# Kernel optimization log

Measured on AMD Instinct MI355X. Metric: run time of the kernel, lower is better.

Reference implementation:

```python
import jax, jax.numpy as jnp
import numpy as np


def setup_inputs() -> dict:
    key = jax.random.key(0)
    k1, k2, k3, k4 = jax.random.split(key, 4)
    B, C, K = 8192, 32000, 100
    return {
        "logits": jax.random.normal(k1, (B, C), dtype=jnp.float32),
        "targets": jax.random.randint(k2, (B,), 0, C, dtype=jnp.int32),
        "text_keys": jax.random.randint(k3, (B,), 0, K, dtype=jnp.int32),
        "class_weight_table": jax.random.uniform(k4, (K, C), dtype=jnp.float32),
    }


def reference(logits, targets, text_keys, class_weight_table):
    # per-sample cross entropy: -log_softmax(logits)[i, targets[i]]
    logp = jax.nn.log_softmax(logits, axis=-1)            # [B, C]
    B = logits.shape[0]
    ce = -jnp.take_along_axis(logp, targets[:, None], axis=-1)[:, 0]  # [B]
    # weight lookup: class_weight[text_key][target]
    w = class_weight_table[text_keys, targets]            # [B]
    return jnp.mean(ce * w)
```

## Files before the change

### kernel.cpp

```cpp
#include <hip/hip_runtime.h>
#include <math.h>


#define L2E 1.44269504088896340736f
#define LN2 0.69314718055994530942f

__device__ __forceinline__ float e2x(float x) {
    return __builtin_amdgcn_exp2f(x * L2E);
}
__device__ __forceinline__ float acc4(float4 v) {
    return (e2x(v.x) + e2x(v.y)) + (e2x(v.z) + e2x(v.w));
}

__global__ __launch_bounds__(256) void row_loss_kernel(
    const float* __restrict__ logits,
    const int*   __restrict__ targets,
    const int*   __restrict__ text_keys,
    const float* __restrict__ wtab,
    float*       __restrict__ row_out,
    int C)
{
    const int row = blockIdx.x;
    const float* rowp = logits + (size_t)row * (size_t)C;
    const int tid = threadIdx.x;

    float xt = 0.0f, wgt = 0.0f;
    if (tid == 0) {
        const int t = targets[row];
        xt  = rowp[t];
        wgt = wtab[(size_t)text_keys[row] * (size_t)C + t];
    }

    const int nvec = C >> 2;
    const float4* rowv = (const float4*)rowp;

    float s0 = 0.0f, s1 = 0.0f, s2 = 0.0f, s3 = 0.0f;

    const int full = nvec >> 10;
    int i = tid;
    if (full > 0) {
        float4 a = rowv[i];
        float4 b = rowv[i + 256];
        float4 c = rowv[i + 512];
        float4 d = rowv[i + 768];
        #pragma unroll 1
        for (int it = 1; it < full; ++it) {
            i += 1024;
            float4 a2 = rowv[i];
            float4 b2 = rowv[i + 256];
            float4 c2 = rowv[i + 512];
            float4 d2 = rowv[i + 768];
            s0 += acc4(a); s1 += acc4(b); s2 += acc4(c); s3 += acc4(d);
            a = a2; b = b2; c = c2; d = d2;
        }
        s0 += acc4(a); s1 += acc4(b); s2 += acc4(c); s3 += acc4(d);
        i += 1024;
    }
    for (; i < nvec; i += 256) s0 += acc4(rowv[i]);
    for (int j = (nvec << 2) + tid; j < C; j += 256) s1 += e2x(rowp[j]);

    float s = (s0 + s1) + (s2 + s3);
    #pragma unroll
    for (int off = 32; off > 0; off >>= 1)
        s += __shfl_down(s, off, 64);

    __shared__ float sm[4];
    const int wave = tid >> 6;
    const int lane = tid & 63;
    if (lane == 0) sm[wave] = s;
    __syncthreads();
    if (tid == 0) {
        const float S = (sm[0] + sm[1]) + (sm[2] + sm[3]);
        const float lse = __builtin_amdgcn_logf(S) * LN2;
        row_out[row] = (lse - xt) * wgt;
    }
}

__global__ __launch_bounds__(256) void reduce_mean_kernel(
    const float* __restrict__ row_out, float* __restrict__ out, int B)
{
    const int tid = threadIdx.x;
    float acc = 0.0f;
    for (int i = tid; i < B; i += 256) acc += row_out[i];
    #pragma unroll
    for (int off = 32; off > 0; off >>= 1)
        acc += __shfl_down(acc, off, 64);
    __shared__ float sa[4];
    const int wave = tid >> 6;
    const int lane = tid & 63;
    if (lane == 0) sa[wave] = acc;
    __syncthreads();
    if (tid == 0) {
        out[0] = (sa[0] + sa[1] + sa[2] + sa[3]) / (float)B;
    }
}

extern "C" void kernel_launch(void* const* d_in, const int* in_sizes, int n_in,
                              void* d_out, int out_size, void* d_ws, size_t ws_size,
                              hipStream_t stream) {
    const float* logits    = (const float*)d_in[0];
    const int*   targets   = (const int*)d_in[1];
    const int*   text_keys = (const int*)d_in[2];
    const float* wtab      = (const float*)d_in[3];
    float* out    = (float*)d_out;
    float* row_ws = (float*)d_ws;

    const int B = in_sizes[1];
    const int C = in_sizes[0] / B;

    row_loss_kernel<<<B, 256, 0, stream>>>(logits, targets, text_keys, wtab,
                                           row_ws, C);
    reduce_mean_kernel<<<1, 256, 0, stream>>>(row_ws, out, B);
}
```

Baseline: 1.300 ms.

## Assign one wavefront per row and use nontemporal vector loads

Each 64-lane wavefront now processes a full row, with four rows per 256-thread block. This removes the shared-memory reduction and the block barrier. The per-row loop now issues four nontemporal float4 loads per lane per iteration, and the software-pipelined prefetch is gone. Each wave streams more data serially per row, which relies on many resident waves to keep memory bandwidth saturated. Nontemporal loads are meant to avoid polluting the cache with streamed logits.

```diff
diff --git a/kernel.cpp b/kernel.cpp
--- a/kernel.cpp
+++ b/kernel.cpp
@@ -5,73 +5,62 @@
 #define L2E 1.44269504088896340736f
 #define LN2 0.69314718055994530942f
 
+typedef __attribute__((ext_vector_type(4))) float f32x4;
+
 __device__ __forceinline__ float e2x(float x) {
     return __builtin_amdgcn_exp2f(x * L2E);
 }
-__device__ __forceinline__ float acc4(float4 v) {
+__device__ __forceinline__ float acc4(f32x4 v) {
     return (e2x(v.x) + e2x(v.y)) + (e2x(v.z) + e2x(v.w));
 }
+__device__ __forceinline__ f32x4 ntload4(const f32x4* p) {
+    return __builtin_nontemporal_load(p);
+}
 
-__global__ __launch_bounds__(256) void row_loss_kernel(
+__global__ __launch_bounds__(256) void row_loss_wave_kernel(
     const float* __restrict__ logits,
     const int*   __restrict__ targets,
     const int*   __restrict__ text_keys,
     const float* __restrict__ wtab,
     float*       __restrict__ row_out,
-    int C)
+    int C, int B)
 {
-    const int row = blockIdx.x;
+    const int wave = threadIdx.x >> 6;
+    const int lane = threadIdx.x & 63;
+    const int row  = (blockIdx.x << 2) + wave;
+    if (row >= B) return;
     const float* rowp = logits + (size_t)row * (size_t)C;
-    const int tid = threadIdx.x;
 
     float xt = 0.0f, wgt = 0.0f;
-    if (tid == 0) {
+    if (lane == 0) {
         const int t = targets[row];
         xt  = rowp[t];
         wgt = wtab[(size_t)text_keys[row] * (size_t)C + t];
     }
 
     const int nvec = C >> 2;
-    const float4* rowv = (const float4*)rowp;
+    const f32x4* rowv = (const f32x4*)rowp;
 
     float s0 = 0.0f, s1 = 0.0f, s2 = 0.0f, s3 = 0.0f;
 
-    const int full = nvec >> 10;
-    int i = tid;
-    if (full > 0) {
-        float4 a = rowv[i];
-        float4 b = rowv[i + 256];
-        float4 c = rowv[i + 512];
-        float4 d = rowv[i + 768];
-        #pragma unroll 1
-        for (int it = 1; it < full; ++it) {
-            i += 1024;
-            float4 a2 = rowv[i];
-            float4 b2 = rowv[i + 256];
-            float4 c2 = rowv[i + 512];
-            float4 d2 = rowv[i + 768];
-            s0 += acc4(a); s1 += acc4(b); s2 += acc4(c); s3 += acc4(d);
-            a = a2; b = b2; c = c2; d = d2;
-        }
+    int i = lane;
+    for (; i + 192 < nvec; i += 256) {
+        f32x4 a = ntload4(rowv + i);
+        f32x4 b = ntload4(rowv + i + 64);
+        f32x4 c = ntload4(rowv + i + 128);
+        f32x4 d = ntload4(rowv + i + 192);
         s0 += acc4(a); s1 += acc4(b); s2 += acc4(c); s3 += acc4(d);
-        i += 1024;
     }
-    for (; i < nvec; i += 256) s0 += acc4(rowv[i]);
-    for (int j = (nvec << 2) + tid; j < C; j += 256) s1 += e2x(rowp[j]);
+    for (; i < nvec; i += 64) s0 += acc4(ntload4(rowv + i));
+    for (int j = (nvec << 2) + lane; j < C; j += 64) s1 += e2x(rowp[j]);
 
     float s = (s0 + s1) + (s2 + s3);
     #pragma unroll
     for (int off = 32; off > 0; off >>= 1)
         s += __shfl_down(s, off, 64);
 
-    __shared__ float sm[4];
-    const int wave = tid >> 6;
-    const int lane = tid & 63;
-    if (lane == 0) sm[wave] = s;
-    __syncthreads();
-    if (tid == 0) {
-        const float S = (sm[0] + sm[1]) + (sm[2] + sm[3]);
-        const float lse = __builtin_amdgcn_logf(S) * LN2;
+    if (lane == 0) {
+        const float lse = __builtin_amdgcn_logf(s) * LN2;
         row_out[row] = (lse - xt) * wgt;
     }
 }
@@ -108,7 +97,8 @@
     const int B = in_sizes[1];
     const int C = in_sizes[0] / B;
 
-    row_loss_kernel<<<B, 256, 0, stream>>>(logits, targets, text_keys, wtab,
-                                           row_ws, C);
+    const int nblk = (B + 3) >> 2;
+    row_loss_wave_kernel<<<nblk, 256, 0, stream>>>(logits, targets, text_keys,
+                                                   wtab, row_ws, C, B);
     reduce_mean_kernel<<<1, 256, 0, stream>>>(row_ws, out, B);
 }
```

Result: faster. 1.259 ms (-3.1%).
